# Kernel tuning notes

Hardware: AMD Instinct MI355X
Metric: run time of the kernel (lower is better)

Reference implementation:

```python
import jax, jax.numpy as jnp
import numpy as np

N, D, K = 65536, 64, 128   # points, feature dim, n_clusters
BETA = 0.0                 # distance weighting exponent offset
EPS = 1e-8


def pairwise_distance(a, b):
    # euclidean distance matrix [n, k]
    d2 = jnp.sum(a * a, 1)[:, None] + jnp.sum(b * b, 1)[None, :] - 2.0 * (a @ b.T)
    return jnp.sqrt(jnp.maximum(d2, 0.0))


def approx_cluster_filling(dist, beta):
    # differentiable soft cluster filling: inverse-distance weights with exponent (1+beta),
    # normalized per point, averaged over points -> [K]
    w = (dist + EPS) ** (-(1.0 + beta))
    w = w / jnp.sum(w, axis=1, keepdims=True)
    return jnp.mean(w, axis=0)


def wasserstein_distance(a, b):
    # sort-based per-feature 1D Wasserstein-1 distance, averaged over features
    return jnp.mean(jnp.abs(jnp.sort(a, axis=0) - jnp.sort(b, axis=0)))


def setup_inputs():
    key = jax.random.key(0)
    k1, k2, k3 = jax.random.split(key, 3)
    x = jax.random.normal(k1, (N, D), jnp.float32)
    target = jax.random.normal(k2, (N, D), jnp.float32)
    cluster_centers = jax.random.normal(k3, (K, D), jnp.float32)
    # precomputed target-side cluster statistics (LossKMeans.__init__, detached)
    dist_t = pairwise_distance(target, cluster_centers)
    prediction_target = jnp.argmin(dist_t, axis=1).astype(jnp.int32)
    filling_target = approx_cluster_filling(dist_t, BETA)
    return {"x": x, "target": target, "cluster_centers": cluster_centers,
            "prediction_target": prediction_target, "filling_target": filling_target}


def reference(x, target, cluster_centers, prediction_target, filling_target):
    # cluster-filling MSE (differentiable soft assignment)
    dist_x = pairwise_distance(x, cluster_centers)
    loss_fil = jnp.mean((approx_cluster_filling(dist_x, BETA) - filling_target) ** 2)
    # hard (detached) cluster assignment of x; concrete in eager mode
    pred_x = np.asarray(jnp.argmin(dist_x, axis=1))
    pred_t = np.asarray(prediction_target)
    loss_med = jnp.zeros((), jnp.float32)
    for c in np.unique(pred_x):  # data-dependent loop over occupied clusters (<= K)
        ix = np.nonzero(pred_x == c)[0]
        it = np.nonzero(pred_t == c)[0]
        m = min(ix.size, it.size)
        if m == 0:
            continue  # no matching target members -> skip (empty slices)
        loss_med = loss_med + wasserstein_distance(x[ix[:m]], target[it[:m]])
    return loss_fil + loss_med
```

## Files before the change

### kernel.cpp

```cpp
#include <hip/hip_runtime.h>
#include <math.h>

#define N_PTS 65536
#define DIM   64
#define K_CL  128
#define EPSV  1e-8f
#define CAP   8192


__global__ __launch_bounds__(256) void k_init(
    float* __restrict__ fill_acc, float* __restrict__ sumw,
    unsigned long long* __restrict__ pred_enc) {
  const int i = blockIdx.x * 256 + threadIdx.x;
  if (i < K_CL) fill_acc[i] = 0.0f;
  sumw[i] = 0.0f;
  pred_enc[i] = 0xFFFFFFFFFFFFFFFFull;
}

__global__ __launch_bounds__(256) void k_dist1(
    const float* __restrict__ x, const float* __restrict__ centers,
    float* __restrict__ sumw, unsigned long long* __restrict__ pred_enc,
    float* __restrict__ w)
{
  __shared__ float csq[32];
  const int kb    = blockIdx.x & 3;
  const int pb    = blockIdx.x >> 2;
  const int jbase = kb << 5;
  const int tid   = threadIdx.x;
  const int p     = pb * 256 + tid;

  if (tid < 32) {
    const float* cp = centers + (jbase + tid) * DIM;
    float s = 0.0f;
    #pragma unroll 8
    for (int d = 0; d < DIM; ++d) { float v = cp[d]; s += v * v; }
    csq[tid] = s;
  }

  float xr[DIM];
  const float4* xp = reinterpret_cast<const float4*>(x + (size_t)p * DIM);
  #pragma unroll
  for (int q = 0; q < DIM / 4; ++q) {
    float4 v = xp[q];
    xr[4 * q + 0] = v.x; xr[4 * q + 1] = v.y;
    xr[4 * q + 2] = v.z; xr[4 * q + 3] = v.w;
  }
  float xsq = 0.0f;
  #pragma unroll
  for (int d = 0; d < DIM; ++d) xsq += xr[d] * xr[d];
  __syncthreads();

  float sw = 0.0f, best = INFINITY;
  int   bj = jbase;
  #pragma unroll 2
  for (int jj = 0; jj < 32; ++jj) {
    const int j = jbase + jj;
    const float* cp = centers + j * DIM;
    float d0 = 0.f, d1 = 0.f, d2a = 0.f, d3 = 0.f;
    #pragma unroll
    for (int d = 0; d < DIM; d += 4) {
      d0  += xr[d + 0] * cp[d + 0];
      d1  += xr[d + 1] * cp[d + 1];
      d2a += xr[d + 2] * cp[d + 2];
      d3  += xr[d + 3] * cp[d + 3];
    }
    float dot  = (d0 + d1) + (d2a + d3);
    float dsq  = xsq + csq[jj] - 2.0f * dot;
    float dist = sqrtf(fmaxf(dsq, 0.0f));
    float ww   = 1.0f / (dist + EPSV);
    w[(size_t)j * N_PTS + p] = ww;
    sw += ww;
    if (dist < best) { best = dist; bj = j; }
  }
  atomicAdd(&sumw[p], sw);
  const unsigned long long enc =
      ((unsigned long long)__float_as_uint(best) << 32) | (unsigned int)bj;
  atomicMin(&pred_enc[p], enc);
}

__global__ __launch_bounds__(256) void k_pred(
    const unsigned long long* __restrict__ pred_enc,
    const float* __restrict__ sumw,
    int* __restrict__ pred_x, float* __restrict__ inv_sumw) {
  const int p = blockIdx.x * 256 + threadIdx.x;
  pred_x[p]   = (int)(pred_enc[p] & 0xFFFFFFFFull);
  inv_sumw[p] = 1.0f / sumw[p];
}

__global__ __launch_bounds__(256) void k_fill(
    const float* __restrict__ w, const float* __restrict__ inv_sumw,
    float* __restrict__ fill_acc)
{
  __shared__ float red[4];
  const int j    = blockIdx.x >> 3;
  const int seg  = blockIdx.x & 7;
  const int tid  = threadIdx.x;
  const float4* wj = reinterpret_cast<const float4*>(
      w + (size_t)j * N_PTS + seg * 8192);
  const float4* iv = reinterpret_cast<const float4*>(inv_sumw + seg * 8192);
  float s = 0.0f;
  #pragma unroll
  for (int q = 0; q < 8; ++q) {
    const int e = q * 256 + tid;
    float4 a = wj[e];
    float4 b = iv[e];
    s += a.x * b.x + a.y * b.y + a.z * b.z + a.w * b.w;
  }
  #pragma unroll
  for (int off = 32; off > 0; off >>= 1) s += __shfl_down(s, off);
  if ((tid & 63) == 0) red[tid >> 6] = s;
  __syncthreads();
  if (tid == 0)
    atomicAdd(&fill_acc[j], red[0] + red[1] + red[2] + red[3]);
}

__global__ __launch_bounds__(1024) void k_scatter(
    const int* __restrict__ pred_x, const int* __restrict__ pred_t,
    int* __restrict__ idx_x, int* __restrict__ idx_t,
    int* __restrict__ count_x, int* __restrict__ count_t)
{
  const int c    = blockIdx.x >> 1;
  const int side = blockIdx.x & 1;
  const int* __restrict__ pred = side ? pred_t : pred_x;
  int* __restrict__ out = side ? idx_t : idx_x;
  int* __restrict__ cnt = side ? count_t : count_x;

  __shared__ int wsum[16];
  const int tid = threadIdx.x, lane = tid & 63, w = tid >> 6;
  const int beg = w * 4096;

  int cw = 0;
  for (int s = 0; s < 4096; s += 64) {
    const bool m = (pred[beg + s + lane] == c);
    cw += __popcll(__ballot(m));
  }
  if (lane == 0) wsum[w] = cw;
  __syncthreads();
  int base = 0, tot = 0;
  #pragma unroll
  for (int k = 0; k < 16; ++k) { int v = wsum[k]; tot += v; if (k < w) base += v; }

  int run = base;
  for (int s = 0; s < 4096; s += 64) {
    const int i = beg + s + lane;
    const bool m = (pred[i] == c);
    unsigned long long bal = __ballot(m);
    int lp = __popcll(bal & ((1ull << lane) - 1ull));
    if (m) { int pos = run + lp; if (pos < CAP) out[c * CAP + pos] = i; }
    run += __popcll(bal);
  }
  if (tid == 0) cnt[c] = tot;
}

__global__ __launch_bounds__(128) void k_offsets(
    const int* __restrict__ count_x, const int* __restrict__ count_t,
    int* __restrict__ offc, int* __restrict__ ord)
{
  __shared__ int sm[128];
  __shared__ int mm[128];
  const int tid = threadIdx.x;
  const int m  = min(min(count_x[tid], CAP), min(count_t[tid], CAP));
  const int sz = ((m + 3) & ~3) * DIM;
  sm[tid] = sz;
  mm[tid] = m;
  __syncthreads();
  int rank = 0;
  for (int j = 0; j < 128; ++j) {
    const int mj = mm[j];
    if (mj > m || (mj == m && j < tid)) ++rank;
  }
  ord[rank] = tid;
  for (int s = 1; s < 128; s <<= 1) {
    int v = (tid >= s) ? sm[tid - s] : 0;
    __syncthreads();
    sm[tid] += v;
    __syncthreads();
  }
  offc[tid] = sm[tid] - sz;
}

__global__ __launch_bounds__(256) void k_gather_t(
    const float* __restrict__ x, const float* __restrict__ t,
    const int* __restrict__ idx_x, const int* __restrict__ idx_t,
    const int* __restrict__ count_x, const int* __restrict__ count_t,
    const int* __restrict__ offc,
    float* __restrict__ gxT, float* __restrict__ gtT)
{
  const int wid  = blockIdx.x * 4 + (threadIdx.x >> 6);
  const int lane = threadIdx.x & 63;
  const int side = wid >> 14;
  const int c    = (wid >> 7) & 127;
  const int q    = wid & 127;
  const int m = min(min(count_x[c], CAP), min(count_t[c], CAP));
  if (q * 64 >= m) return;
  const int r  = q * 64 + lane;
  const int mp = (m + 3) & ~3;
  const float* __restrict__ src = side ? t : x;
  const int*   __restrict__ idx = side ? idx_t : idx_x;
  float* __restrict__ dst = (side ? gtT : gxT) + offc[c];
  if (r < m) {
    const float4* rp =
        reinterpret_cast<const float4*>(src + (size_t)idx[c * CAP + r] * DIM);
    float v[DIM];
    #pragma unroll
    for (int qq = 0; qq < DIM / 4; ++qq) {
      float4 f = rp[qq];
      v[4*qq+0]=f.x; v[4*qq+1]=f.y; v[4*qq+2]=f.z; v[4*qq+3]=f.w;
    }
    #pragma unroll
    for (int d = 0; d < DIM; ++d) dst[(size_t)d * mp + r] = v[d];
  }
}

__device__ __forceinline__ void ce(float& a, float& b, bool up) {
  float lo = fminf(a, b), hi = fmaxf(a, b);
  a = up ? lo : hi;
  b = up ? hi : lo;
}

__device__ __forceinline__ void merge8(float* v, bool up) {
  ce(v[0],v[4],up); ce(v[1],v[5],up); ce(v[2],v[6],up); ce(v[3],v[7],up);
  ce(v[0],v[2],up); ce(v[1],v[3],up); ce(v[4],v[6],up); ce(v[5],v[7],up);
  ce(v[0],v[1],up); ce(v[2],v[3],up); ce(v[4],v[5],up); ce(v[6],v[7],up);
}

__device__ __forceinline__ void sort8(float* v, bool up8) {
  ce(v[0],v[1],true );  ce(v[2],v[3],false); ce(v[4],v[5],true );  ce(v[6],v[7],false);
  ce(v[0],v[2],true );  ce(v[1],v[3],true );  ce(v[4],v[6],false); ce(v[5],v[7],false);
  ce(v[0],v[1],true );  ce(v[2],v[3],true );  ce(v[4],v[5],false); ce(v[6],v[7],false);
  merge8(v, up8);
}

__device__ __forceinline__ void merge16(float* v, bool up) {
  #pragma unroll
  for (int e = 0; e < 8; ++e) ce(v[e], v[e + 8], up);
  merge8(v, up);
  merge8(v + 8, up);
}

__device__ __forceinline__ void sort16(float* v, bool up16) {
  sort8(v, true);
  sort8(v + 8, false);
  merge16(v, up16);
}

__device__ __forceinline__ void stage_one8(float v[8], int ib, int k, bool up) {
  for (int j = (k >> 1) > 256 ? 256 : (k >> 1); j >= 8; j >>= 1) {
    const int  jl = j >> 3;
    const bool tm = (up == ((ib & j) == 0));
    float p[8];
    #pragma unroll
    for (int e = 0; e < 8; ++e) p[e] = __shfl_xor(v[e], jl, 64);
    if (tm) {
      #pragma unroll
      for (int e = 0; e < 8; ++e) v[e] = fminf(v[e], p[e]);
    } else {
      #pragma unroll
      for (int e = 0; e < 8; ++e) v[e] = fmaxf(v[e], p[e]);
    }
  }
  merge8(v, up);
}

__device__ __forceinline__ void stage_one16(float v[16], int ib, int k, bool up) {
  #pragma unroll
  for (int j = (k >> 1) > 512 ? 512 : (k >> 1); j >= 16; j >>= 1) {
    const int  jl = j >> 4;
    const bool tm = (up == ((ib & j) == 0));
    float p[16];
    #pragma unroll
    for (int e = 0; e < 16; ++e) p[e] = __shfl_xor(v[e], jl, 64);
    if (tm) {
      #pragma unroll
      for (int e = 0; e < 16; ++e) v[e] = fminf(v[e], p[e]);
    } else {
      #pragma unroll
      for (int e = 0; e < 16; ++e) v[e] = fmaxf(v[e], p[e]);
    }
  }
  merge16(v, up);
}

__device__ __forceinline__ void load8c(const float* __restrict__ col,
                                       int ib, int m, float v[8]) {
  if (ib + 7 < m) {
    #pragma unroll
    for (int q = 0; q < 2; ++q) {
      float4 f = *(const float4*)&col[ib + 4 * q];
      v[4*q+0]=f.x; v[4*q+1]=f.y; v[4*q+2]=f.z; v[4*q+3]=f.w;
    }
  } else {
    #pragma unroll
    for (int e = 0; e < 8; ++e) v[e] = (ib + e < m) ? col[ib + e] : INFINITY;
  }
}

__device__ __forceinline__ void load16c(const float* __restrict__ col,
                                        int ib, int m, float v[16]) {
  if (ib + 15 < m) {
    #pragma unroll
    for (int q = 0; q < 4; ++q) {
      float4 f = *(const float4*)&col[ib + 4 * q];
      v[4*q+0]=f.x; v[4*q+1]=f.y; v[4*q+2]=f.z; v[4*q+3]=f.w;
    }
  } else {
    #pragma unroll
    for (int e = 0; e < 16; ++e) v[e] = (ib + e < m) ? col[ib + e] : INFINITY;
  }
}

__device__ __forceinline__ int swz4(int fi) {
  return fi ^ (((fi >> 5) & 7) << 2);
}

template<int P>
__device__ __forceinline__ void sort_col(float v[16], int ib, bool act,
                                         const float* __restrict__ col,
                                         int m, float* __restrict__ sa) {
  if (act) {
    load16c(col, ib, m, v);
    sort16(v, ((ib & 16) == 0));
    #pragma unroll
    for (int k = 32; k <= 1024; k <<= 1)
      stage_one16(v, ib, k, ((ib & k) == 0));
  }
  #pragma unroll
  for (int k = 2048; k <= P; k <<= 1) {
    const bool up = ((ib & k) == 0);
    #pragma unroll
    for (int j = k >> 1; j >= 1024; j >>= 1) {
      __syncthreads();
      if (act) {
        #pragma unroll
        for (int q = 0; q < 4; ++q)
          *(float4*)&sa[swz4(ib + 4*q)] =
              make_float4(v[4*q], v[4*q+1], v[4*q+2], v[4*q+3]);
      }
      __syncthreads();
      if (act) {
        const int pi = ib ^ j;
        const bool tm = (up == ((ib & j) == 0));
        float A[16];
        #pragma unroll
        for (int q = 0; q < 4; ++q) {
          float4 f = *(const float4*)&sa[swz4(pi + 4*q)];
          A[4*q+0]=f.x; A[4*q+1]=f.y; A[4*q+2]=f.z; A[4*q+3]=f.w;
        }
        if (tm) {
          #pragma unroll
          for (int e = 0; e < 16; ++e) v[e] = fminf(v[e], A[e]);
        } else {
          #pragma unroll
          for (int e = 0; e < 16; ++e) v[e] = fmaxf(v[e], A[e]);
        }
      }
    }
    if (act) stage_one16(v, ib, k, up);
  }
}

template<int P>
__device__ __forceinline__ void sort_col_io(float* __restrict__ col,
                                            int m, int mp, int tid,
                                            float* __restrict__ sa) {
  const int ib = tid << 4;
  const bool act = (ib < P);
  float v[16];
  sort_col<P>(v, ib, act, col, m, sa);
  if (act) {
    #pragma unroll
    for (int q = 0; q < 4; ++q)
      if (ib + 4 * q < mp)
        *(float4*)&col[ib + 4*q] =
            make_float4(v[4*q], v[4*q+1], v[4*q+2], v[4*q+3]);
  }
}

__global__ __launch_bounds__(512) void k_sort(
    float* __restrict__ gxT, float* __restrict__ gtT,
    const int* __restrict__ offc,
    const int* __restrict__ count_x, const int* __restrict__ count_t,
    const int* __restrict__ ord)
{
  __shared__ float sa[8192];
  const int tid = threadIdx.x;

  if (blockIdx.x < 16384) {
    const int side = blockIdx.x >> 13;
    const int cd   = blockIdx.x & 8191;
    const int c = ord[cd >> 6], d = cd & 63;
    const int m = min(min(count_x[c], CAP), min(count_t[c], CAP));
    if (m <= 1024) return;
    const int mp = (m + 3) & ~3;
    float* col = (side ? gtT : gxT) + offc[c] + (size_t)d * mp;
    if (m <= 2048)      sort_col_io<2048>(col, m, mp, tid, sa);
    else if (m <= 4096) sort_col_io<4096>(col, m, mp, tid, sa);
    else                sort_col_io<8192>(col, m, mp, tid, sa);
  } else {
    const int base = (blockIdx.x - 16384) * 8 + (tid >> 6);
    const int lane = tid & 63;
    const int side = base >> 13;
    const int cd   = base & 8191;
    const int c = ord[cd >> 6], d = cd & 63;
    const int m = min(min(count_x[c], CAP), min(count_t[c], CAP));
    if (m > 1024 || m == 0) return;
    const int mp = (m + 3) & ~3;
    float* col = (side ? gtT : gxT) + offc[c] + (size_t)d * mp;

    if (m <= 512) {
      int P = 8;
      while (P < m) P <<= 1;
      const int ib = lane << 3;
      float v[8];
      load8c(col, ib, m, v);
      sort8(v, ((ib & 8) == 0));
      for (int k = 16; k <= P; k <<= 1)
        stage_one8(v, ib, k, ((ib & k) == 0));
      #pragma unroll
      for (int q = 0; q < 2; ++q)
        if (ib + 4 * q < mp)
          *(float4*)&col[ib + 4*q] =
              make_float4(v[4*q], v[4*q+1], v[4*q+2], v[4*q+3]);
    } else {
      const int ib = lane << 4;
      float v[16];
      load16c(col, ib, m, v);
      sort16(v, ((ib & 16) == 0));
      #pragma unroll
      for (int k = 32; k <= 1024; k <<= 1)
        stage_one16(v, ib, k, ((ib & k) == 0));
      #pragma unroll
      for (int q = 0; q < 4; ++q)
        if (ib + 4 * q < mp)
          *(float4*)&col[ib + 4*q] =
              make_float4(v[4*q], v[4*q+1], v[4*q+2], v[4*q+3]);
    }
  }
}

__global__ __launch_bounds__(256) void k_diff(
    const float* __restrict__ gxT, const float* __restrict__ gtT,
    const int* __restrict__ offc,
    const int* __restrict__ count_x, const int* __restrict__ count_t,
    float* __restrict__ parts)
{
  __shared__ float red[4];
  const int task = blockIdx.x;
  const int c = task >> 6, d = task & 63;
  const int m = min(min(count_x[c], CAP), min(count_t[c], CAP));
  const int tid = threadIdx.x;
  if (m == 0) { if (tid == 0) parts[task] = 0.0f; return; }
  const int mp = (m + 3) & ~3;
  const float* colx = gxT + offc[c] + (size_t)d * mp;
  const float* colt = gtT + offc[c] + (size_t)d * mp;
  float s = 0.0f;
  for (int r = tid * 4; r < mp; r += 1024) {
    float4 a = *(const float4*)&colx[r];
    float4 b = *(const float4*)&colt[r];
    if (r + 3 < m) {
      s += fabsf(a.x-b.x) + fabsf(a.y-b.y) + fabsf(a.z-b.z) + fabsf(a.w-b.w);
    } else {
      if (r + 0 < m) s += fabsf(a.x - b.x);
      if (r + 1 < m) s += fabsf(a.y - b.y);
      if (r + 2 < m) s += fabsf(a.z - b.z);
      if (r + 3 < m) s += fabsf(a.w - b.w);
    }
  }
  #pragma unroll
  for (int off = 32; off > 0; off >>= 1) s += __shfl_down(s, off);
  if ((tid & 63) == 0) red[tid >> 6] = s;
  __syncthreads();
  if (tid == 0)
    parts[task] = (red[0] + red[1] + red[2] + red[3]) / (float)(m * DIM);
}

__global__ __launch_bounds__(1024) void k_final(
    const float* __restrict__ fill_acc, const float* __restrict__ ft,
    const float* __restrict__ parts, float* __restrict__ out)
{
  __shared__ float red[16];
  const int tid = threadIdx.x;
  float s = 0.0f;
  #pragma unroll
  for (int i = 0; i < 8; ++i) s += parts[tid + i * 1024];
  if (tid < K_CL) {
    float v = fill_acc[tid] * (1.0f / (float)N_PTS) - ft[tid];
    s += v * v * (1.0f / (float)K_CL);
  }
  #pragma unroll
  for (int off = 32; off > 0; off >>= 1) s += __shfl_down(s, off);
  if ((tid & 63) == 0) red[tid >> 6] = s;
  __syncthreads();
  if (tid == 0) {
    float tot = 0.0f;
    #pragma unroll
    for (int w = 0; w < 16; ++w) tot += red[w];
    out[0] = tot;
  }
}

extern "C" void kernel_launch(void* const* d_in, const int* in_sizes, int n_in,
                              void* d_out, int out_size, void* d_ws, size_t ws_size,
                              hipStream_t stream)
{
  (void)in_sizes; (void)n_in; (void)out_size; (void)ws_size;
  const float* x      = (const float*)d_in[0];
  const float* target = (const float*)d_in[1];
  const float* cc     = (const float*)d_in[2];
  const int*   pred_t = (const int*)d_in[3];
  const float* ft     = (const float*)d_in[4];
  float* out = (float*)d_out;

  char* ws = (char*)d_ws;
  float* fill_acc = (float*)(ws + 0);
  int*   pred_x   = (int*)(ws + 1024);
  int*   idx_x    = (int*)(ws + 263168);
  int*   idx_t    = (int*)(ws + 4457472);
  int*   count_x  = (int*)(ws + 8651776);
  int*   count_t  = (int*)(ws + 8651776 + 512);
  float* parts    = (float*)(ws + 8652800);
  float* sumw     = (float*)(ws + 8685568);
  float* inv_sumw = (float*)(ws + 8947712);
  unsigned long long* pred_enc = (unsigned long long*)(ws + 9209856);
  int*   offc     = (int*)(ws + 9734144);
  int*   ord      = (int*)(ws + 9734656);
  float* gxT      = (float*)(ws + 9735168);
  float* gtT      = (float*)(ws + 26643456);
  float* wmat     = (float*)(ws + 9735168);

  k_init<<<N_PTS / 256, 256, 0, stream>>>(fill_acc, sumw, pred_enc);
  k_dist1<<<N_PTS / 256 * 4, 256, 0, stream>>>(x, cc, sumw, pred_enc, wmat);
  k_pred<<<N_PTS / 256, 256, 0, stream>>>(pred_enc, sumw, pred_x, inv_sumw);
  k_fill<<<K_CL * 8, 256, 0, stream>>>(wmat, inv_sumw, fill_acc);
  k_scatter<<<K_CL * 2, 1024, 0, stream>>>(pred_x, pred_t, idx_x, idx_t,
                                           count_x, count_t);
  k_offsets<<<1, 128, 0, stream>>>(count_x, count_t, offc, ord);
  k_gather_t<<<8192, 256, 0, stream>>>(x, target, idx_x, idx_t,
                                       count_x, count_t, offc, gxT, gtT);
  k_sort<<<16384 + 2048, 512, 0, stream>>>(gxT, gtT, offc, count_x, count_t,
                                           ord);
  k_diff<<<K_CL * DIM, 256, 0, stream>>>(gxT, gtT, offc,
                                         count_x, count_t, parts);
  k_final<<<1, 1024, 0, stream>>>(fill_acc, ft, parts, out);
}
```

Measured before the change: 316.0 us.

## Fuse distance, argmin and soft filling into one kernel with distance recompute

Replaces the four-kernel front end (init, split-K distance, pred, fill) with one kernel in which each thread handles a point across all 128 centers. The kernel computes the row sum and argmin in a first pass, then recomputes the distances in a second pass to build the normalized weights. These are reduced per wave with shuffles into shared memory, and one atomic per cluster is issued per block. This removes the 32 MB weight-matrix write and read and the per-point atomics. In exchange it doubles the distance FLOPs and cuts the grid to 256 blocks, which lowers parallelism.

Result: slower. 405.0 us (+28.2%).

```diff
diff --git a/kernel.cpp b/kernel.cpp
--- a/kernel.cpp
+++ b/kernel.cpp
@@ -8,34 +8,28 @@
 #define CAP   8192
 
 
-__global__ __launch_bounds__(256) void k_init(
-    float* __restrict__ fill_acc, float* __restrict__ sumw,
-    unsigned long long* __restrict__ pred_enc) {
-  const int i = blockIdx.x * 256 + threadIdx.x;
-  if (i < K_CL) fill_acc[i] = 0.0f;
-  sumw[i] = 0.0f;
-  pred_enc[i] = 0xFFFFFFFFFFFFFFFFull;
-}
-
-__global__ __launch_bounds__(256) void k_dist1(
+__global__ __launch_bounds__(128) void k_init0(float* __restrict__ fill_acc) {
+  fill_acc[threadIdx.x] = 0.0f;
+}
+
+__global__ __launch_bounds__(256) void k_front(
     const float* __restrict__ x, const float* __restrict__ centers,
-    float* __restrict__ sumw, unsigned long long* __restrict__ pred_enc,
-    float* __restrict__ w)
-{
-  __shared__ float csq[32];
-  const int kb    = blockIdx.x & 3;
-  const int pb    = blockIdx.x >> 2;
-  const int jbase = kb << 5;
-  const int tid   = threadIdx.x;
-  const int p     = pb * 256 + tid;
-
-  if (tid < 32) {
-    const float* cp = centers + (jbase + tid) * DIM;
+    int* __restrict__ pred_x, float* __restrict__ fill_acc)
+{
+  __shared__ float csq[K_CL];
+  __shared__ float wsumf[4 * K_CL];
+  const int tid = threadIdx.x;
+  const int p   = blockIdx.x * 256 + tid;
+
+  if (tid < K_CL) {
+    const float* cp = centers + tid * DIM;
     float s = 0.0f;
     #pragma unroll 8
     for (int d = 0; d < DIM; ++d) { float v = cp[d]; s += v * v; }
     csq[tid] = s;
   }
+  wsumf[tid]       = 0.0f;
+  wsumf[tid + 256] = 0.0f;
 
   float xr[DIM];
   const float4* xp = reinterpret_cast<const float4*>(x + (size_t)p * DIM);
@@ -51,10 +45,9 @@
   __syncthreads();
 
   float sw = 0.0f, best = INFINITY;
-  int   bj = jbase;
+  int   bj = 0;
   #pragma unroll 2
-  for (int jj = 0; jj < 32; ++jj) {
-    const int j = jbase + jj;
+  for (int j = 0; j < K_CL; ++j) {
     const float* cp = centers + j * DIM;
     float d0 = 0.f, d1 = 0.f, d2a = 0.f, d3 = 0.f;
     #pragma unroll
@@ -65,53 +58,40 @@
       d3  += xr[d + 3] * cp[d + 3];
     }
     float dot  = (d0 + d1) + (d2a + d3);
-    float dsq  = xsq + csq[jj] - 2.0f * dot;
+    float dsq  = xsq + csq[j] - 2.0f * dot;
     float dist = sqrtf(fmaxf(dsq, 0.0f));
     float ww   = 1.0f / (dist + EPSV);
-    w[(size_t)j * N_PTS + p] = ww;
     sw += ww;
     if (dist < best) { best = dist; bj = j; }
   }
-  atomicAdd(&sumw[p], sw);
-  const unsigned long long enc =
-      ((unsigned long long)__float_as_uint(best) << 32) | (unsigned int)bj;
-  atomicMin(&pred_enc[p], enc);
-}
-
-__global__ __launch_bounds__(256) void k_pred(
-    const unsigned long long* __restrict__ pred_enc,
-    const float* __restrict__ sumw,
-    int* __restrict__ pred_x, float* __restrict__ inv_sumw) {
-  const int p = blockIdx.x * 256 + threadIdx.x;
-  pred_x[p]   = (int)(pred_enc[p] & 0xFFFFFFFFull);
-  inv_sumw[p] = 1.0f / sumw[p];
-}
-
-__global__ __launch_bounds__(256) void k_fill(
-    const float* __restrict__ w, const float* __restrict__ inv_sumw,
-    float* __restrict__ fill_acc)
-{
-  __shared__ float red[4];
-  const int j    = blockIdx.x >> 3;
-  const int seg  = blockIdx.x & 7;
-  const int tid  = threadIdx.x;
-  const float4* wj = reinterpret_cast<const float4*>(
-      w + (size_t)j * N_PTS + seg * 8192);
-  const float4* iv = reinterpret_cast<const float4*>(inv_sumw + seg * 8192);
-  float s = 0.0f;
-  #pragma unroll
-  for (int q = 0; q < 8; ++q) {
-    const int e = q * 256 + tid;
-    float4 a = wj[e];
-    float4 b = iv[e];
-    s += a.x * b.x + a.y * b.y + a.z * b.z + a.w * b.w;
-  }
-  #pragma unroll
-  for (int off = 32; off > 0; off >>= 1) s += __shfl_down(s, off);
-  if ((tid & 63) == 0) red[tid >> 6] = s;
+  pred_x[p] = bj;
+  const float inv = 1.0f / sw;
+
+  const int wv = tid >> 6;
+  #pragma unroll 2
+  for (int j = 0; j < K_CL; ++j) {
+    const float* cp = centers + j * DIM;
+    float d0 = 0.f, d1 = 0.f, d2a = 0.f, d3 = 0.f;
+    #pragma unroll
+    for (int d = 0; d < DIM; d += 4) {
+      d0  += xr[d + 0] * cp[d + 0];
+      d1  += xr[d + 1] * cp[d + 1];
+      d2a += xr[d + 2] * cp[d + 2];
+      d3  += xr[d + 3] * cp[d + 3];
+    }
+    float dot  = (d0 + d1) + (d2a + d3);
+    float dsq  = xsq + csq[j] - 2.0f * dot;
+    float dist = sqrtf(fmaxf(dsq, 0.0f));
+    float val  = (1.0f / (dist + EPSV)) * inv;
+    #pragma unroll
+    for (int off = 32; off > 0; off >>= 1) val += __shfl_down(val, off);
+    if ((tid & 63) == 0) wsumf[wv * K_CL + j] += val;
+  }
   __syncthreads();
-  if (tid == 0)
-    atomicAdd(&fill_acc[j], red[0] + red[1] + red[2] + red[3]);
+  if (tid < K_CL)
+    atomicAdd(&fill_acc[tid],
+              (wsumf[tid] + wsumf[K_CL + tid]) +
+              (wsumf[2 * K_CL + tid] + wsumf[3 * K_CL + tid]));
 }
 
 __global__ __launch_bounds__(1024) void k_scatter(
@@ -519,19 +499,13 @@
   int*   count_x  = (int*)(ws + 8651776);
   int*   count_t  = (int*)(ws + 8651776 + 512);
   float* parts    = (float*)(ws + 8652800);
-  float* sumw     = (float*)(ws + 8685568);
-  float* inv_sumw = (float*)(ws + 8947712);
-  unsigned long long* pred_enc = (unsigned long long*)(ws + 9209856);
   int*   offc     = (int*)(ws + 9734144);
   int*   ord      = (int*)(ws + 9734656);
   float* gxT      = (float*)(ws + 9735168);
   float* gtT      = (float*)(ws + 26643456);
-  float* wmat     = (float*)(ws + 9735168);
-
-  k_init<<<N_PTS / 256, 256, 0, stream>>>(fill_acc, sumw, pred_enc);
-  k_dist1<<<N_PTS / 256 * 4, 256, 0, stream>>>(x, cc, sumw, pred_enc, wmat);
-  k_pred<<<N_PTS / 256, 256, 0, stream>>>(pred_enc, sumw, pred_x, inv_sumw);
-  k_fill<<<K_CL * 8, 256, 0, stream>>>(wmat, inv_sumw, fill_acc);
+
+  k_init0<<<1, 128, 0, stream>>>(fill_acc);
+  k_front<<<N_PTS / 256, 256, 0, stream>>>(x, cc, pred_x, fill_acc);
   k_scatter<<<K_CL * 2, 1024, 0, stream>>>(pred_x, pred_t, idx_x, idx_t,
                                            count_x, count_t);
   k_offsets<<<1, 128, 0, stream>>>(count_x, count_t, offc, ord);
```
